# Kernel optimization log

Hardware: AMD Instinct MI355X
Metric: run time of the kernel (lower is better)

Reference implementation:

```python
import jax, jax.numpy as jnp
import numpy as np

B, S, CIN = 16384, 24, 10
NH, DK, DM = 16, 8, 256
DV = DM // NH  # 16
EPS = 1e-5
T_POS = 1000.0


def _ln(x, g, b):
    mu = jnp.mean(x, axis=-1, keepdims=True)
    var = jnp.mean((x - mu) ** 2, axis=-1, keepdims=True)
    return (x - mu) * jax.lax.rsqrt(var + EPS) * g + b


def _bn(x, g, b, m, v):
    # eval-mode BatchNorm1d over channel (last) dim
    return (x - m) * jax.lax.rsqrt(v + EPS) * g + b


def setup_inputs() -> dict:
    key = jax.random.key(0)
    ks = jax.random.split(key, 16)
    x = jax.random.normal(ks[0], (B, S, CIN + 1), dtype=jnp.float32)
    pos = jax.random.uniform(ks[1], (B, S), dtype=jnp.float32) * 365.0
    x = x.at[:, :, 0].set(pos)
    w = lambda k, shp, s=0.05: (jax.random.normal(k, shp, dtype=jnp.float32) * s)
    d = {
        'x': x,
        'ln1_g': jnp.ones((CIN,), jnp.float32), 'ln1_b': jnp.zeros((CIN,), jnp.float32),
        'conv_w': w(ks[2], (DM, CIN)), 'conv_b': jnp.zeros((DM,), jnp.float32),
        'bn1_g': jnp.ones((DM,), jnp.float32), 'bn1_b': jnp.zeros((DM,), jnp.float32),
        'bn1_m': jnp.zeros((DM,), jnp.float32), 'bn1_v': jnp.ones((DM,), jnp.float32),
        'Q': w(ks[3], (NH, DK), float(np.sqrt(2.0 / DK))),
        'Wk': w(ks[4], (NH * DK, DM), float(np.sqrt(2.0 / DK))), 'bk': jnp.zeros((NH * DK,), jnp.float32),
        'W1': w(ks[5], (128, 256)), 'b1': jnp.zeros((128,), jnp.float32),
        'bn2_g': jnp.ones((128,), jnp.float32), 'bn2_b': jnp.zeros((128,), jnp.float32),
        'bn2_m': jnp.zeros((128,), jnp.float32), 'bn2_v': jnp.ones((128,), jnp.float32),
        'oln_g': jnp.ones((128,), jnp.float32), 'oln_b': jnp.zeros((128,), jnp.float32),
        'Wd1': w(ks[6], (64, 128)), 'bd1': jnp.zeros((64,), jnp.float32),
        'bnd1_g': jnp.ones((64,), jnp.float32), 'bnd1_b': jnp.zeros((64,), jnp.float32),
        'bnd1_m': jnp.zeros((64,), jnp.float32), 'bnd1_v': jnp.ones((64,), jnp.float32),
        'Wd2': w(ks[7], (32, 64)), 'bd2': jnp.zeros((32,), jnp.float32),
        'bnd2_g': jnp.ones((32,), jnp.float32), 'bnd2_b': jnp.zeros((32,), jnp.float32),
        'bnd2_m': jnp.zeros((32,), jnp.float32), 'bnd2_v': jnp.ones((32,), jnp.float32),
        'Wd3': w(ks[8], (20, 32)), 'bd3': jnp.zeros((20,), jnp.float32),
    }
    return d


def reference(x, ln1_g, ln1_b, conv_w, conv_b, bn1_g, bn1_b, bn1_m, bn1_v,
              Q, Wk, bk, W1, b1, bn2_g, bn2_b, bn2_m, bn2_v, oln_g, oln_b,
              Wd1, bd1, bnd1_g, bnd1_b, bnd1_m, bnd1_v,
              Wd2, bd2, bnd2_g, bnd2_b, bnd2_m, bnd2_v, Wd3, bd3):
    pos = x[:, :, 0]            # (B, S) positions
    feat = x[:, :, 1:]          # (B, S, CIN)
    feat = _ln(feat, ln1_g, ln1_b)
    # inconv: 1x1 Conv1d == per-timestep Linear, then eval BatchNorm1d over channels
    h = jnp.einsum('bsc,dc->bsd', feat, conv_w) + conv_b
    h = _bn(h, bn1_g, bn1_b, bn1_m, bn1_v)
    # sinusoid positional encoding, interleaved sin/cos
    div = jnp.exp(jnp.arange(0, DM, 2, dtype=jnp.float32) * (-np.log(T_POS) / DM))  # (DM/2,)
    ang = pos[:, :, None] * div                                   # (B, S, DM/2)
    pe = jnp.stack([jnp.sin(ang), jnp.cos(ang)], axis=-1).reshape(pos.shape[0], pos.shape[1], DM)
    e = h + pe                                                    # (B, S, DM)
    # LTAE multi-head attention with shared learned query
    k = jnp.einsum('bsd,hkd->bshk', e, Wk.reshape(NH, DK, DM)) + bk.reshape(NH, DK)
    logits = jnp.einsum('hk,bshk->bhs', Q, k) / np.sqrt(DK)
    attn = jax.nn.softmax(logits, axis=-1)                        # (B, NH, S); dropout=eval
    v = e.reshape(e.shape[0], e.shape[1], NH, DV)                 # head-chunked values
    o = jnp.einsum('bhs,bshc->bhc', attn, v).reshape(e.shape[0], NH * DV)  # (B, 256)
    # MLP3: Linear(256,128) + BN + ReLU, then dropout(eval) + LayerNorm
    m = jax.nn.relu(_bn(o @ W1.T + b1, bn2_g, bn2_b, bn2_m, bn2_v))
    m = _ln(m, oln_g, oln_b)
    # decoder: [128,64,32,20]
    d1 = jax.nn.relu(_bn(m @ Wd1.T + bd1, bnd1_g, bnd1_b, bnd1_m, bnd1_v))
    d2 = jax.nn.relu(_bn(d1 @ Wd2.T + bd2, bnd2_g, bnd2_b, bnd2_m, bnd2_v))
    out = d2 @ Wd3.T + bd3                                        # (B, 20)
    return out
```

## Files before the change

### kernel.cpp

```cpp
#include <hip/hip_runtime.h>
#include <hip/hip_bf16.h>


typedef __attribute__((ext_vector_type(8))) short bf16x8;
typedef __attribute__((ext_vector_type(4))) float f32x4;

#define EPS 1e-5f
#define INV_SQRT8 0.35355339059327373f
#define KDIV (-0.07785768972392256f)
#define INV2PI 0.15915494309189535f
#define LOG2E 1.4426950408889634f

__device__ __forceinline__ unsigned short f2bf(float f){
  union { float f; unsigned u; } v; v.f = f;
  unsigned r = v.u + 0x7FFFu + ((v.u >> 16) & 1u);
  return (unsigned short)(r >> 16);
}
__device__ __forceinline__ float bf2f(unsigned short h){
  union { unsigned u; float f; } v; v.u = ((unsigned)h) << 16; return v.f;
}
__device__ __forceinline__ unsigned pk2bf(float lo, float hi){
  __hip_bfloat162 h2 = __float22bfloat162_rn(make_float2(lo, hi));
  return *reinterpret_cast<unsigned*>(&h2);
}

__global__ __launch_bounds__(256) void k0_pre(
    const float* __restrict__ conv_w, const float* __restrict__ conv_b,
    const float* __restrict__ bn1_g, const float* __restrict__ bn1_b,
    const float* __restrict__ bn1_m, const float* __restrict__ bn1_v,
    const float* __restrict__ Q, const float* __restrict__ Wk,
    const float* __restrict__ bk,
    const float* __restrict__ W1, const float* __restrict__ b1,
    const float* __restrict__ bn2_g, const float* __restrict__ bn2_b,
    const float* __restrict__ bn2_m, const float* __restrict__ bn2_v,
    const float* __restrict__ oln_g, const float* __restrict__ oln_b,
    const float* __restrict__ Wd1, const float* __restrict__ bd1,
    const float* __restrict__ bnd1_g, const float* __restrict__ bnd1_b,
    const float* __restrict__ bnd1_m, const float* __restrict__ bnd1_v,
    const float* __restrict__ Wd2, const float* __restrict__ bd2,
    const float* __restrict__ bnd2_g, const float* __restrict__ bnd2_b,
    const float* __restrict__ bnd2_m, const float* __restrict__ bnd2_v,
    const float* __restrict__ Wd3,
    unsigned short* __restrict__ wqF, unsigned short* __restrict__ w1F,
    unsigned short* __restrict__ wd1F, unsigned short* __restrict__ wd2F,
    unsigned short* __restrict__ wd3F,
    float* __restrict__ convwT, float* __restrict__ convbE,
    float* __restrict__ biasq, float* __restrict__ b1E,
    float* __restrict__ bd1E, float* __restrict__ bd2E)
{
  __shared__ float redL[256];
  const int t = threadIdx.x;
  const int bid = blockIdx.x;

  if (bid < 64){
    for (int e = bid*512 + t; e < bid*512 + 512; e += 256){
      int j = e & 7, lj = (e >> 3) & 63, kc = (e >> 9) & 7, nt = (e >> 12) & 7;
      int n = nt*16 + (lj & 15);
      int k = kc*32 + ((lj >> 4) << 3) + j;
      float s2 = bn2_g[n] * rsqrtf(bn2_v[n] + EPS);
      w1F[e] = f2bf(W1[n*256 + k] * s2);
    }
  } else if (bid < 68){
    int base = (bid - 64)*2048;
    #pragma unroll 4
    for (int it = 0; it < 8; ++it){
      int e = base + it*256 + t;
      int j = e & 7, lj = (e >> 3) & 63, kc = (e >> 9) & 3, nt = (e >> 11) & 3;
      int n = nt*16 + (lj & 15);
      int k = kc*32 + ((lj >> 4) << 3) + j;
      float sd = bnd1_g[n] * rsqrtf(bnd1_v[n] + EPS);
      wd1F[e] = f2bf(Wd1[n*128 + k] * sd * oln_g[k]);
    }
  } else if (bid == 68){
    #pragma unroll 4
    for (int it = 0; it < 8; ++it){
      int e = it*256 + t;
      int j = e & 7, lj = (e >> 3) & 63, kc = (e >> 9) & 1, nt = (e >> 10) & 1;
      int n = nt*16 + (lj & 15);
      int k = kc*32 + ((lj >> 4) << 3) + j;
      float sd = bnd2_g[n] * rsqrtf(bnd2_v[n] + EPS);
      wd2F[e] = f2bf(Wd2[n*64 + k] * sd);
    }
  } else if (bid == 69){
    #pragma unroll
    for (int it = 0; it < 4; ++it){
      int e = it*256 + t;
      int j = e & 7, lj = (e >> 3) & 63, nt = (e >> 9) & 1;
      int n = nt*16 + (lj & 15);
      int k = ((lj >> 4) << 3) + j;
      float v = (n < 20) ? Wd3[n*32 + k] : 0.f;
      wd3F[e] = f2bf(v);
    }
  } else if (bid == 70){
    #pragma unroll 4
    for (int it = 0; it < 16; ++it){
      int e = it*256 + t;
      int j = e & 7, lj = (e >> 3) & 63, kc = (e >> 9) & 7;
      int h = lj & 15;
      int dd = kc*32 + ((lj >> 4) << 3) + j;
      float acc = 0.f;
      #pragma unroll
      for (int kk = 0; kk < 8; ++kk)
        acc += Q[h*8+kk] * Wk[(h*8+kk)*256 + dd];
      wqF[e] = f2bf(acc * INV_SQRT8);
    }
  } else if (bid == 71){
    __shared__ float wqL[16*256];
    __shared__ float coefL[256*12];
    __shared__ float QL[128];
    __shared__ float bkL[128];
    wqF[4096 + t] = 0; wqF[4096 + 256 + t] = 0;
    if (t < 128){ QL[t] = Q[t]; bkL[t] = bk[t]; }
    __syncthreads();
    {
      const int d = t;
      float s1 = bn1_g[d] * rsqrtf(bn1_v[d] + EPS);
      #pragma unroll
      for (int c = 0; c < 10; ++c) coefL[d*12 + c] = conv_w[d*10 + c] * s1;
      coefL[d*12 + 10] = conv_b[d]*s1 + bn1_b[d] - bn1_m[d]*s1;
      coefL[d*12 + 11] = 0.f;
      #pragma unroll 4
      for (int h = 0; h < 16; ++h){
        float acc = 0.f;
        #pragma unroll
        for (int kk = 0; kk < 8; ++kk)
          acc += QL[h*8+kk] * Wk[(h*8+kk)*256 + d];
        wqL[h*256 + d] = acc;
      }
    }
    __syncthreads();
    if (t < 176){
      int h = t / 11, cc = t - h*11;
      const float* wq = wqL + h*256;
      float acc = 0.f;
      #pragma unroll 4
      for (int d2 = 0; d2 < 256; ++d2)
        acc += coefL[d2*12 + cc] * wq[d2];
      acc *= INV_SQRT8;
      if (cc < 10){
        int lane = (cc < 8) ? h : (16 + h);
        int j = cc & 7;
        wqF[4096 + lane*8 + j] = f2bf(acc);
      } else {
        float qb = 0.f;
        #pragma unroll
        for (int kk = 0; kk < 8; ++kk) qb += QL[h*8+kk]*bkL[h*8+kk];
        biasq[h] = acc + qb * INV_SQRT8;
      }
    }
  } else if (bid == 72){
    #pragma unroll
    for (int it = 0; it < 10; ++it){
      int e = it*256 + t;
      int c = e >> 8, d = e & 255;
      float s1 = bn1_g[d] * rsqrtf(bn1_v[d] + EPS);
      convwT[e] = conv_w[d*10 + c] * s1;
    }
  } else if (bid == 73){
    {
      int d = t;
      float s1 = bn1_g[d] * rsqrtf(bn1_v[d] + EPS);
      convbE[d] = conv_b[d]*s1 + bn1_b[d] - bn1_m[d]*s1;
    }
    if (t < 128){
      float s2 = bn2_g[t] * rsqrtf(bn2_v[t] + EPS);
      b1E[t] = b1[t]*s2 + bn2_b[t] - bn2_m[t]*s2;
    }
    if (t < 32){
      float sd = bnd2_g[t] * rsqrtf(bnd2_v[t] + EPS);
      bd2E[t] = bd2[t]*sd + bnd2_b[t] - bnd2_m[t]*sd;
    }
  } else {
    int n = t >> 2, si = t & 3;
    float acc = 0.f;
    #pragma unroll 8
    for (int i2 = 0; i2 < 32; ++i2){
      int i = si*32 + i2;
      acc += oln_b[i] * Wd1[n*128 + i];
    }
    redL[t] = acc;
    __syncthreads();
    if (t < 64){
      float sd = bnd1_g[t] * rsqrtf(bnd1_v[t] + EPS);
      float a = redL[4*t] + redL[4*t+1] + redL[4*t+2] + redL[4*t+3];
      bd1E[t] = bd1[t]*sd + bnd1_b[t] - bnd1_m[t]*sd + a*sd;
    }
  }
}

__global__ __launch_bounds__(256, 4) void k1_attn(
    const float* __restrict__ x, const float* __restrict__ ln1_g,
    const float* __restrict__ ln1_b,
    const unsigned short* __restrict__ wqF, const float* __restrict__ convwT,
    const float* __restrict__ convbE, const float* __restrict__ biasq,
    unsigned short* __restrict__ o_ws)
{
  __shared__ unsigned short peR[48*264];
  __shared__ unsigned short featn[48*16];
  __shared__ float attnF[2*16*28];
  __shared__ float shmix[384];
  __shared__ __align__(16) unsigned short zeroB[8];
  float* posL = shmix;
  float* divL = shmix + 64;
  float* gL   = shmix;

  const int t = threadIdx.x;
  const int b0 = blockIdx.x * 2;
  const int w = t >> 6, l = t & 63;

  if (t < 128) divL[t] = exp2f((float)t * KDIV) * INV2PI;
  if (t < 8) zeroB[t] = 0;

  if (t < 48){
    int bb = t >= 24; int s = t - bb*24;
    const float* xr = x + ((size_t)(b0+bb)*24 + s)*11;
    float f[10]; float mu = 0.f;
    #pragma unroll
    for (int c = 0; c < 10; ++c){ f[c] = xr[1+c]; mu += f[c]; }
    posL[t] = xr[0];
    mu *= 0.1f;
    float var = 0.f;
    #pragma unroll
    for (int c = 0; c < 10; ++c){ float dv = f[c]-mu; var += dv*dv; }
    var *= 0.1f;
    float rs = rsqrtf(var + EPS);
    float fn[10];
    #pragma unroll
    for (int c = 0; c < 10; ++c) fn[c] = (f[c]-mu)*rs*ln1_g[c] + ln1_b[c];
    #pragma unroll
    for (int q = 0; q < 5; ++q)
      *(unsigned*)(featn + t*16 + 2*q) = pk2bf(fn[2*q], fn[2*q+1]);
    #pragma unroll
    for (int z = 0; z < 3; ++z)
      *(unsigned*)(featn + t*16 + 10 + 2*z) = 0u;
  }
  __syncthreads();

  {
    const int g = (l >> 4) & 3, rlo = l & 15;
    #pragma unroll
    for (int it = 0; it < 6; ++it){
      int combo = it*4 + w;
      int mt = combo >> 3, kc = combo & 7;
      int row = mt*16 + rlo;
      int run = kc*4 + g;
      float p = posL[row];
      unsigned pk[4];
      #pragma unroll
      for (int q = 0; q < 4; ++q){
        float dv = divL[run*4 + q];
        float ang = p * dv;
        float fr = ang - floorf(ang);
        float sv = __builtin_amdgcn_sinf(fr);
        float cv = __builtin_amdgcn_cosf(fr);
        pk[q] = pk2bf(sv, cv);
      }
      *(uint4*)(peR + row*264 + run*8) = make_uint4(pk[0], pk[1], pk[2], pk[3]);
    }
  }
  __syncthreads();

  {
    if (w < 3){
      const int mt = w;
      const int m = l & 15, g = l >> 4;
      f32x4 acc = {0.f,0.f,0.f,0.f};
      #pragma unroll
      for (int kc = 0; kc < 8; ++kc){
        bf16x8 a = *(const bf16x8*)(peR + (mt*16 + m)*264 + kc*32 + g*8);
        bf16x8 b = *(const bf16x8*)(wqF + ((size_t)(kc*64 + l))*8);
        acc = __builtin_amdgcn_mfma_f32_16x16x32_bf16(a, b, acc, 0, 0, 0);
      }
      {
        const unsigned short* ap = (g < 2) ? (featn + (mt*16 + m)*16 + g*8)
                                           : zeroB;
        bf16x8 a = *(const bf16x8*)ap;
        bf16x8 b = *(const bf16x8*)(wqF + ((size_t)(8*64 + l))*8);
        acc = __builtin_amdgcn_mfma_f32_16x16x32_bf16(a, b, acc, 0, 0, 0);
      }
      const int h = m;
      float bq = biasq[h];
      #pragma unroll
      for (int reg = 0; reg < 4; ++reg){
        int row = mt*16 + g*4 + reg;
        int bb = row >= 24; int s = row - bb*24;
        attnF[(bb*16+h)*28 + s] = acc[reg] + bq;
      }
    }
  }
  __syncthreads();

  if (t < 32){
    float* L = attnF + t*28;
    float mx = -1e30f;
    for (int s = 0; s < 24; ++s) mx = fmaxf(mx, L[s]);
    float sum = 0.f;
    for (int s = 0; s < 24; ++s){
      float p = exp2f((L[s]-mx)*LOG2E); L[s] = p; sum += p;
    }
    float inv = 1.f / sum;
    for (int s = 0; s < 24; ++s) L[s] *= inv;
  }
  __syncthreads();

  if (t < 160){
    int bb = t / 80; int rem = t - bb*80;
    int h = rem / 5, c = rem - h*5;
    const float* A = attnF + (bb*16+h)*28;
    float g0 = 0.f, g1 = 0.f;
    for (int s = 0; s < 24; ++s){
      float a = A[s];
      const unsigned short* fr = featn + (bb*24+s)*16;
      g0 += a * bf2f(fr[c]);
      g1 += a * bf2f(fr[c+5]);
    }
    gL[(bb*16+h)*12 + c]     = g0;
    gL[(bb*16+h)*12 + c + 5] = g1;
  }
  __syncthreads();

  {
    const int d = t, h = d >> 4;
    float cw[10];
    #pragma unroll
    for (int c = 0; c < 10; ++c) cw[c] = convwT[c*256 + d];
    float cb = convbE[d];
    #pragma unroll
    for (int bb = 0; bb < 2; ++bb){
      float o = cb;
      const float* gp = gL + (bb*16+h)*12;
      #pragma unroll
      for (int c = 0; c < 10; ++c) o += cw[c]*gp[c];
      const float* A = attnF + (bb*16+h)*28;
      const unsigned short* pr = peR + (bb*24)*264 + d;
      #pragma unroll
      for (int s = 0; s < 24; ++s)
        o += A[s] * bf2f(pr[s*264]);
      o_ws[(size_t)(b0+bb)*256 + d] = f2bf(o);
    }
  }
}

__global__ __launch_bounds__(256, 4) void k2_mlp(
    const unsigned short* __restrict__ o_ws,
    const unsigned short* __restrict__ w1F, const float* __restrict__ b1E,
    const unsigned short* __restrict__ wd1F, const float* __restrict__ bd1E,
    const unsigned short* __restrict__ wd2F, const float* __restrict__ bd2E,
    const unsigned short* __restrict__ wd3F, const float* __restrict__ bd3,
    float* __restrict__ out)
{
  __shared__ float mL[16*132];
  __shared__ unsigned short mh[16*136];
  __shared__ unsigned short d1L[16*72];
  __shared__ unsigned short d2L[16*40];
  __shared__ float redL[64];
  __shared__ float stats[32];

  const int t = threadIdx.x;
  const int w = t >> 6, l = t & 63;
  const size_t rowBase = (size_t)blockIdx.x * 16;
  const int g8  = (l >> 4) << 3;
  const int c15 = l & 15;

  {
    f32x4 acc[2];
    { f32x4 z = {0.f,0.f,0.f,0.f}; acc[0] = z; acc[1] = z; }
    #pragma unroll
    for (int kc = 0; kc < 8; ++kc){
      bf16x8 a = *(const bf16x8*)(o_ws + (rowBase + c15)*256 + kc*32 + g8);
      #pragma unroll
      for (int n2 = 0; n2 < 2; ++n2){
        int nt = 2*w + n2;
        bf16x8 b = *(const bf16x8*)(w1F + ((size_t)((nt*8+kc)*64 + l))*8);
        acc[n2] = __builtin_amdgcn_mfma_f32_16x16x32_bf16(a, b, acc[n2], 0,0,0);
      }
    }
    #pragma unroll
    for (int n2 = 0; n2 < 2; ++n2){
      int col = (2*w + n2)*16 + c15;
      float be = b1E[col];
      #pragma unroll
      for (int reg = 0; reg < 4; ++reg){
        int row = ((l>>4)<<2) + reg;
        mL[row*132 + col] = fmaxf(acc[n2][reg] + be, 0.f);
      }
    }
  }
  __syncthreads();

  if (t < 32){
    const float* R = mL + (t>>1)*132 + (t&1)*64;
    float s = 0.f, q = 0.f;
    for (int k = 0; k < 64; ++k){ float v = R[k]; s += v; q += v*v; }
    redL[t*2] = s; redL[t*2+1] = q;
  }
  __syncthreads();
  if (t < 16){
    float s = redL[4*t] + redL[4*t+2];
    float q = redL[4*t+1] + redL[4*t+3];
    float mu = s * (1.f/128.f);
    float var = q * (1.f/128.f) - mu*mu;
    stats[2*t] = mu; stats[2*t+1] = rsqrtf(var + EPS);
  }
  __syncthreads();

  {
    int r = t >> 4, run = t & 15;
    float mu = stats[2*r], rs = stats[2*r+1];
    const float* R = mL + r*132 + run*8;
    unsigned pk[4];
    #pragma unroll
    for (int q = 0; q < 4; ++q)
      pk[q] = pk2bf((R[2*q]-mu)*rs, (R[2*q+1]-mu)*rs);
    *(uint4*)(mh + r*136 + run*8) = make_uint4(pk[0], pk[1], pk[2], pk[3]);
  }
  __syncthreads();

  {
    const int nt = w;
    f32x4 acc = {0.f,0.f,0.f,0.f};
    #pragma unroll
    for (int kc = 0; kc < 4; ++kc){
      bf16x8 b = *(const bf16x8*)(wd1F + ((size_t)((nt*4+kc)*64 + l))*8);
      bf16x8 a = *(const bf16x8*)(mh + c15*136 + kc*32 + g8);
      acc = __builtin_amdgcn_mfma_f32_16x16x32_bf16(a, b, acc, 0,0,0);
    }
    int col = nt*16 + c15;
    float be = bd1E[col];
    #pragma unroll
    for (int reg = 0; reg < 4; ++reg){
      int row = ((l>>4)<<2) + reg;
      d1L[row*72 + col] = f2bf(fmaxf(acc[reg] + be, 0.f));
    }
  }
  __syncthreads();

  if (w < 2){
    const int nt = w;
    f32x4 acc = {0.f,0.f,0.f,0.f};
    #pragma unroll
    for (int kc = 0; kc < 2; ++kc){
      bf16x8 a = *(const bf16x8*)(d1L + c15*72 + kc*32 + g8);
      bf16x8 b = *(const bf16x8*)(wd2F + ((size_t)((nt*2+kc)*64 + l))*8);
      acc = __builtin_amdgcn_mfma_f32_16x16x32_bf16(a, b, acc, 0,0,0);
    }
    int col = nt*16 + c15;
    float be = bd2E[col];
    #pragma unroll
    for (int reg = 0; reg < 4; ++reg){
      int row = ((l>>4)<<2) + reg;
      d2L[row*40 + col] = f2bf(fmaxf(acc[reg] + be, 0.f));
    }
  }
  __syncthreads();

  if (w < 2){
    const int nt = w;
    bf16x8 a = *(const bf16x8*)(d2L + c15*40 + g8);
    bf16x8 b = *(const bf16x8*)(wd3F + ((size_t)(nt*64 + l))*8);
    f32x4 acc = {0.f,0.f,0.f,0.f};
    acc = __builtin_amdgcn_mfma_f32_16x16x32_bf16(a, b, acc, 0,0,0);
    int col = nt*16 + c15;
    if (col < 20){
      float be = bd3[col];
      #pragma unroll
      for (int reg = 0; reg < 4; ++reg){
        int row = ((l>>4)<<2) + reg;
        out[(rowBase + row)*20 + col] = acc[reg] + be;
      }
    }
  }
}

extern "C" void kernel_launch(void* const* d_in, const int* in_sizes, int n_in,
                              void* d_out, int out_size, void* d_ws, size_t ws_size,
                              hipStream_t stream)
{
  (void)in_sizes; (void)n_in; (void)out_size; (void)ws_size;
  const float* x      = (const float*)d_in[0];
  const float* ln1_g  = (const float*)d_in[1];
  const float* ln1_b  = (const float*)d_in[2];
  const float* conv_w = (const float*)d_in[3];
  const float* conv_b = (const float*)d_in[4];
  const float* bn1_g  = (const float*)d_in[5];
  const float* bn1_b  = (const float*)d_in[6];
  const float* bn1_m  = (const float*)d_in[7];
  const float* bn1_v  = (const float*)d_in[8];
  const float* Q      = (const float*)d_in[9];
  const float* Wk     = (const float*)d_in[10];
  const float* bk     = (const float*)d_in[11];
  const float* W1     = (const float*)d_in[12];
  const float* b1     = (const float*)d_in[13];
  const float* bn2_g  = (const float*)d_in[14];
  const float* bn2_b  = (const float*)d_in[15];
  const float* bn2_m  = (const float*)d_in[16];
  const float* bn2_v  = (const float*)d_in[17];
  const float* oln_g  = (const float*)d_in[18];
  const float* oln_b  = (const float*)d_in[19];
  const float* Wd1    = (const float*)d_in[20];
  const float* bd1    = (const float*)d_in[21];
  const float* bnd1_g = (const float*)d_in[22];
  const float* bnd1_b = (const float*)d_in[23];
  const float* bnd1_m = (const float*)d_in[24];
  const float* bnd1_v = (const float*)d_in[25];
  const float* Wd2    = (const float*)d_in[26];
  const float* bd2    = (const float*)d_in[27];
  const float* bnd2_g = (const float*)d_in[28];
  const float* bnd2_b = (const float*)d_in[29];
  const float* bnd2_m = (const float*)d_in[30];
  const float* bnd2_v = (const float*)d_in[31];
  const float* Wd3    = (const float*)d_in[32];
  const float* bd3    = (const float*)d_in[33];

  char* ws = (char*)d_ws;
  unsigned short* wqF  = (unsigned short*)(ws + 0);
  unsigned short* w1F  = (unsigned short*)(ws + 9216);
  unsigned short* wd1F = (unsigned short*)(ws + 74752);
  unsigned short* wd2F = (unsigned short*)(ws + 91136);
  unsigned short* wd3F = (unsigned short*)(ws + 95232);
  float* convwT = (float*)(ws + 97280);
  float* convbE = (float*)(ws + 107520);
  float* biasq  = (float*)(ws + 108544);
  float* b1E    = (float*)(ws + 108608);
  float* bd1E   = (float*)(ws + 109120);
  float* bd2E   = (float*)(ws + 109376);
  unsigned short* o_ws = (unsigned short*)(ws + 109568);

  hipLaunchKernelGGL(k0_pre, dim3(75), dim3(256), 0, stream,
      conv_w, conv_b, bn1_g, bn1_b, bn1_m, bn1_v, Q, Wk, bk,
      W1, b1, bn2_g, bn2_b, bn2_m, bn2_v, oln_g, oln_b,
      Wd1, bd1, bnd1_g, bnd1_b, bnd1_m, bnd1_v,
      Wd2, bd2, bnd2_g, bnd2_b, bnd2_m, bnd2_v, Wd3,
      wqF, w1F, wd1F, wd2F, wd3F, convwT, convbE, biasq, b1E, bd1E, bd2E);

  hipLaunchKernelGGL(k1_attn, dim3(8192), dim3(256), 0, stream,
      x, ln1_g, ln1_b, wqF, convwT, convbE, biasq, o_ws);

  hipLaunchKernelGGL(k2_mlp, dim3(1024), dim3(256), 0, stream,
      o_ws, w1F, b1E, wd1F, bd1E, wd2F, bd2E, wd3F, bd3, (float*)d_out);
}
```

Before: 193.5 us.

## Fuse PE generation into MFMA loop, coalesce x load, parallelize softmax, fragment-layout output

The attention kernel now loads each block's x rows with a coalesced float4 copy into shared memory. LayerNorm runs on a separate wave while the other three waves compute positional-encoding fragments and feed them straight into the MFMA accumulation, saving a barrier and an LDS reload. Softmax is spread over all 256 threads with shuffle reductions instead of 32 serial threads. The final weighted sum processes two channels per thread with packed bf16 loads. The output is written in the MFMA fragment layout that k2 reads directly. Smaller changes pad shared arrays to cut bank conflicts, at the cost of more complex indexing and strided, less coalesced writes to o_frag.

```diff
diff --git a/kernel.cpp b/kernel.cpp
--- a/kernel.cpp
+++ b/kernel.cpp
@@ -18,6 +18,9 @@
 }
 __device__ __forceinline__ float bf2f(unsigned short h){
   union { unsigned u; float f; } v; v.u = ((unsigned)h) << 16; return v.f;
+}
+__device__ __forceinline__ float asf(unsigned u){
+  union { unsigned u; float f; } v; v.u = u; return v.f;
 }
 __device__ __forceinline__ unsigned pk2bf(float lo, float hi){
   __hip_bfloat162 h2 = __float22bfloat162_rn(make_float2(lo, hi));
@@ -105,7 +108,7 @@
       wqF[e] = f2bf(acc * INV_SQRT8);
     }
   } else if (bid == 71){
-    __shared__ float wqL[16*256];
+    __shared__ float wqL[16*257];
     __shared__ float coefL[256*12];
     __shared__ float QL[128];
     __shared__ float bkL[128];
@@ -125,13 +128,13 @@
         #pragma unroll
         for (int kk = 0; kk < 8; ++kk)
           acc += QL[h*8+kk] * Wk[(h*8+kk)*256 + d];
-        wqL[h*256 + d] = acc;
+        wqL[h*257 + d] = acc;
       }
     }
     __syncthreads();
     if (t < 176){
       int h = t / 11, cc = t - h*11;
-      const float* wq = wqL + h*256;
+      const float* wq = wqL + h*257;
       float acc = 0.f;
       #pragma unroll 4
       for (int d2 = 0; d2 < 256; ++d2)
@@ -193,120 +196,122 @@
     const float* __restrict__ ln1_b,
     const unsigned short* __restrict__ wqF, const float* __restrict__ convwT,
     const float* __restrict__ convbE, const float* __restrict__ biasq,
-    unsigned short* __restrict__ o_ws)
+    unsigned short* __restrict__ o_frag)
 {
   __shared__ unsigned short peR[48*264];
+  __shared__ float attnF[2*16*25];
   __shared__ unsigned short featn[48*16];
-  __shared__ float attnF[2*16*28];
-  __shared__ float shmix[384];
+  __shared__ float xL[528];
+  __shared__ float divL[128];
   __shared__ __align__(16) unsigned short zeroB[8];
-  float* posL = shmix;
-  float* divL = shmix + 64;
-  float* gL   = shmix;
+  float* gL = xL;
 
   const int t = threadIdx.x;
   const int b0 = blockIdx.x * 2;
   const int w = t >> 6, l = t & 63;
 
+  if (t < 132)
+    *(float4*)(xL + t*4) = *(const float4*)(x + (size_t)b0*264 + t*4);
   if (t < 128) divL[t] = exp2f((float)t * KDIV) * INV2PI;
   if (t < 8) zeroB[t] = 0;
-
-  if (t < 48){
-    int bb = t >= 24; int s = t - bb*24;
-    const float* xr = x + ((size_t)(b0+bb)*24 + s)*11;
-    float f[10]; float mu = 0.f;
-    #pragma unroll
-    for (int c = 0; c < 10; ++c){ f[c] = xr[1+c]; mu += f[c]; }
-    posL[t] = xr[0];
-    mu *= 0.1f;
-    float var = 0.f;
-    #pragma unroll
-    for (int c = 0; c < 10; ++c){ float dv = f[c]-mu; var += dv*dv; }
-    var *= 0.1f;
-    float rs = rsqrtf(var + EPS);
-    float fn[10];
-    #pragma unroll
-    for (int c = 0; c < 10; ++c) fn[c] = (f[c]-mu)*rs*ln1_g[c] + ln1_b[c];
-    #pragma unroll
-    for (int q = 0; q < 5; ++q)
-      *(unsigned*)(featn + t*16 + 2*q) = pk2bf(fn[2*q], fn[2*q+1]);
-    #pragma unroll
-    for (int z = 0; z < 3; ++z)
-      *(unsigned*)(featn + t*16 + 10 + 2*z) = 0u;
-  }
-  __syncthreads();
-
-  {
-    const int g = (l >> 4) & 3, rlo = l & 15;
-    #pragma unroll
-    for (int it = 0; it < 6; ++it){
-      int combo = it*4 + w;
-      int mt = combo >> 3, kc = combo & 7;
-      int row = mt*16 + rlo;
-      int run = kc*4 + g;
-      float p = posL[row];
+  __syncthreads();
+
+  if (w == 3){
+    if (l < 48){
+      const float* xr = xL + l*11;
+      float f[10]; float mu = 0.f;
+      #pragma unroll
+      for (int c = 0; c < 10; ++c){ f[c] = xr[1+c]; mu += f[c]; }
+      mu *= 0.1f;
+      float var = 0.f;
+      #pragma unroll
+      for (int c = 0; c < 10; ++c){ float dv = f[c]-mu; var += dv*dv; }
+      var *= 0.1f;
+      float rs = rsqrtf(var + EPS);
+      float fn[10];
+      #pragma unroll
+      for (int c = 0; c < 10; ++c) fn[c] = (f[c]-mu)*rs*ln1_g[c] + ln1_b[c];
+      #pragma unroll
+      for (int q = 0; q < 5; ++q)
+        *(unsigned*)(featn + l*16 + 2*q) = pk2bf(fn[2*q], fn[2*q+1]);
+      #pragma unroll
+      for (int z = 0; z < 3; ++z)
+        *(unsigned*)(featn + l*16 + 10 + 2*z) = 0u;
+    }
+  }
+
+  f32x4 acc = {0.f,0.f,0.f,0.f};
+  const int m = l & 15, g = l >> 4;
+  if (w < 3){
+    const int mt = w;
+    const int row = mt*16 + m;
+    const float p = xL[row*11];
+    #pragma unroll
+    for (int kc = 0; kc < 8; ++kc){
+      float4 dv4 = *(const float4*)(divL + kc*16 + g*4);
       unsigned pk[4];
       #pragma unroll
       for (int q = 0; q < 4; ++q){
-        float dv = divL[run*4 + q];
+        float dv = (q==0)?dv4.x:(q==1)?dv4.y:(q==2)?dv4.z:dv4.w;
         float ang = p * dv;
         float fr = ang - floorf(ang);
         float sv = __builtin_amdgcn_sinf(fr);
         float cv = __builtin_amdgcn_cosf(fr);
         pk[q] = pk2bf(sv, cv);
       }
-      *(uint4*)(peR + row*264 + run*8) = make_uint4(pk[0], pk[1], pk[2], pk[3]);
+      union { bf16x8 v; uint4 u; } af;
+      af.u = make_uint4(pk[0], pk[1], pk[2], pk[3]);
+      *(uint4*)(peR + row*264 + (kc*4+g)*8) = af.u;
+      bf16x8 b = *(const bf16x8*)(wqF + ((size_t)(kc*64 + l))*8);
+      acc = __builtin_amdgcn_mfma_f32_16x16x32_bf16(af.v, b, acc, 0, 0, 0);
+    }
+  }
+  __syncthreads();
+
+  if (w < 3){
+    const int mt = w;
+    {
+      const unsigned short* ap = (g < 2) ? (featn + (mt*16 + m)*16 + g*8)
+                                         : zeroB;
+      bf16x8 a = *(const bf16x8*)ap;
+      bf16x8 b = *(const bf16x8*)(wqF + ((size_t)(8*64 + l))*8);
+      acc = __builtin_amdgcn_mfma_f32_16x16x32_bf16(a, b, acc, 0, 0, 0);
+    }
+    const int h = m;
+    float bq = biasq[h];
+    #pragma unroll
+    for (int reg = 0; reg < 4; ++reg){
+      int row = mt*16 + g*4 + reg;
+      int bb = row >= 24; int s = row - bb*24;
+      attnF[(bb*16+h)*25 + s] = acc[reg] + bq;
     }
   }
   __syncthreads();
 
   {
-    if (w < 3){
-      const int mt = w;
-      const int m = l & 15, g = l >> 4;
-      f32x4 acc = {0.f,0.f,0.f,0.f};
-      #pragma unroll
-      for (int kc = 0; kc < 8; ++kc){
-        bf16x8 a = *(const bf16x8*)(peR + (mt*16 + m)*264 + kc*32 + g*8);
-        bf16x8 b = *(const bf16x8*)(wqF + ((size_t)(kc*64 + l))*8);
-        acc = __builtin_amdgcn_mfma_f32_16x16x32_bf16(a, b, acc, 0, 0, 0);
-      }
-      {
-        const unsigned short* ap = (g < 2) ? (featn + (mt*16 + m)*16 + g*8)
-                                           : zeroB;
-        bf16x8 a = *(const bf16x8*)ap;
-        bf16x8 b = *(const bf16x8*)(wqF + ((size_t)(8*64 + l))*8);
-        acc = __builtin_amdgcn_mfma_f32_16x16x32_bf16(a, b, acc, 0, 0, 0);
-      }
-      const int h = m;
-      float bq = biasq[h];
-      #pragma unroll
-      for (int reg = 0; reg < 4; ++reg){
-        int row = mt*16 + g*4 + reg;
-        int bb = row >= 24; int s = row - bb*24;
-        attnF[(bb*16+h)*28 + s] = acc[reg] + bq;
-      }
-    }
-  }
-  __syncthreads();
-
-  if (t < 32){
-    float* L = attnF + t*28;
-    float mx = -1e30f;
-    for (int s = 0; s < 24; ++s) mx = fmaxf(mx, L[s]);
-    float sum = 0.f;
-    for (int s = 0; s < 24; ++s){
-      float p = exp2f((L[s]-mx)*LOG2E); L[s] = p; sum += p;
-    }
-    float inv = 1.f / sum;
-    for (int s = 0; s < 24; ++s) L[s] *= inv;
+    const int bh = t >> 3, ln = t & 7;
+    float* L = attnF + bh*25;
+    float v0 = L[ln], v1 = L[ln+8], v2 = L[ln+16];
+    float mx = fmaxf(fmaxf(v0, v1), v2);
+    mx = fmaxf(mx, __shfl_xor(mx, 1, 64));
+    mx = fmaxf(mx, __shfl_xor(mx, 2, 64));
+    mx = fmaxf(mx, __shfl_xor(mx, 4, 64));
+    float p0 = exp2f((v0-mx)*LOG2E);
+    float p1 = exp2f((v1-mx)*LOG2E);
+    float p2 = exp2f((v2-mx)*LOG2E);
+    float sm = p0 + p1 + p2;
+    sm += __shfl_xor(sm, 1, 64);
+    sm += __shfl_xor(sm, 2, 64);
+    sm += __shfl_xor(sm, 4, 64);
+    float inv = 1.f / sm;
+    L[ln] = p0*inv; L[ln+8] = p1*inv; L[ln+16] = p2*inv;
   }
   __syncthreads();
 
   if (t < 160){
     int bb = t / 80; int rem = t - bb*80;
     int h = rem / 5, c = rem - h*5;
-    const float* A = attnF + (bb*16+h)*28;
+    const float* A = attnF + (bb*16+h)*25;
     float g0 = 0.f, g1 = 0.f;
     for (int s = 0; s < 24; ++s){
       float a = A[s];
@@ -320,29 +325,35 @@
   __syncthreads();
 
   {
-    const int d = t, h = d >> 4;
-    float cw[10];
-    #pragma unroll
-    for (int c = 0; c < 10; ++c) cw[c] = convwT[c*256 + d];
-    float cb = convbE[d];
-    #pragma unroll
-    for (int bb = 0; bb < 2; ++bb){
-      float o = cb;
-      const float* gp = gL + (bb*16+h)*12;
-      #pragma unroll
-      for (int c = 0; c < 10; ++c) o += cw[c]*gp[c];
-      const float* A = attnF + (bb*16+h)*28;
-      const unsigned short* pr = peR + (bb*24)*264 + d;
-      #pragma unroll
-      for (int s = 0; s < 24; ++s)
-        o += A[s] * bf2f(pr[s*264]);
-      o_ws[(size_t)(b0+bb)*256 + d] = f2bf(o);
-    }
+    const int bb = t >> 7, dp = t & 127;
+    const int d0 = dp*2, h = dp >> 3;
+    float2 o2 = *(const float2*)(convbE + d0);
+    const float* gp = gL + (bb*16+h)*12;
+    #pragma unroll
+    for (int c = 0; c < 10; ++c){
+      float2 cw = *(const float2*)(convwT + c*256 + d0);
+      o2.x += cw.x * gp[c];
+      o2.y += cw.y * gp[c];
+    }
+    const float* A = attnF + (bb*16+h)*25;
+    const unsigned short* pr = peR + bb*24*264 + d0;
+    #pragma unroll
+    for (int s = 0; s < 24; ++s){
+      unsigned u = *(const unsigned*)(pr + s*264);
+      float a = A[s];
+      o2.x += a * asf(u << 16);
+      o2.y += a * asf(u & 0xFFFF0000u);
+    }
+    const int row = b0 + bb;
+    const int rt = row >> 4, mm = row & 15;
+    const int kc = d0 >> 5, gg = (d0 >> 3) & 3, j = d0 & 7;
+    *(unsigned*)(o_frag + ((size_t)((rt*8+kc)*64 + gg*16 + mm))*8 + j)
+        = pk2bf(o2.x, o2.y);
   }
 }
 
 __global__ __launch_bounds__(256, 4) void k2_mlp(
-    const unsigned short* __restrict__ o_ws,
+    const unsigned short* __restrict__ o_frag,
     const unsigned short* __restrict__ w1F, const float* __restrict__ b1E,
     const unsigned short* __restrict__ wd1F, const float* __restrict__ bd1E,
     const unsigned short* __restrict__ wd2F, const float* __restrict__ bd2E,
@@ -359,6 +370,7 @@
   const int t = threadIdx.x;
   const int w = t >> 6, l = t & 63;
   const size_t rowBase = (size_t)blockIdx.x * 16;
+  const int rt = blockIdx.x;
   const int g8  = (l >> 4) << 3;
   const int c15 = l & 15;
 
@@ -367,7 +379,7 @@
     { f32x4 z = {0.f,0.f,0.f,0.f}; acc[0] = z; acc[1] = z; }
     #pragma unroll
     for (int kc = 0; kc < 8; ++kc){
-      bf16x8 a = *(const bf16x8*)(o_ws + (rowBase + c15)*256 + kc*32 + g8);
+      bf16x8 a = *(const bf16x8*)(o_frag + ((size_t)((rt*8+kc)*64 + l))*8);
       #pragma unroll
       for (int n2 = 0; n2 < 2; ++n2){
         int nt = 2*w + n2;
@@ -524,7 +536,7 @@
   float* b1E    = (float*)(ws + 108608);
   float* bd1E   = (float*)(ws + 109120);
   float* bd2E   = (float*)(ws + 109376);
-  unsigned short* o_ws = (unsigned short*)(ws + 109568);
+  unsigned short* o_frag = (unsigned short*)(ws + 109568);
 
   hipLaunchKernelGGL(k0_pre, dim3(75), dim3(256), 0, stream,
       conv_w, conv_b, bn1_g, bn1_b, bn1_m, bn1_v, Q, Wk, bk,
@@ -534,8 +546,8 @@
       wqF, w1F, wd1F, wd2F, wd3F, convwT, convbE, biasq, b1E, bd1E, bd2E);
 
   hipLaunchKernelGGL(k1_attn, dim3(8192), dim3(256), 0, stream,
-      x, ln1_g, ln1_b, wqF, convwT, convbE, biasq, o_ws);
+      x, ln1_g, ln1_b, wqF, convwT, convbE, biasq, o_frag);
 
   hipLaunchKernelGGL(k2_mlp, dim3(1024), dim3(256), 0, stream,
-      o_ws, w1F, b1E, wd1F, bd1E, wd2F, bd2E, wd3F, bd3, (float*)d_out);
-}
+      o_frag, w1F, b1E, wd1F, bd1E, wd2F, bd2E, wd3F, bd3, (float*)d_out);
+}
```

Measured after the change: 186.0 us. -3.9%, faster.
